# Optimization experiments

Measured on AMD Instinct MI355X. Metric: run time of the kernel, lower is better.

Reference implementation:

```python
import jax, jax.numpy as jnp
import numpy as np

B, S, D, H = 4, 2048, 1024, 16
DK = D // H
NEG = -1.0e9

def setup_inputs() -> dict:
    key = jax.random.key(0)
    ks = jax.random.split(key, 9)
    scale = 1.0 / np.sqrt(D)
    x = jax.random.normal(ks[0], (B, S, D), dtype=jnp.float32)
    # causal mask: positions with mask==0 are filled with -1e9
    mask = jnp.tril(jnp.ones((S, S), dtype=jnp.int32))[None, None]  # [1,1,S,S]
    Wq = jax.random.normal(ks[1], (D, D), dtype=jnp.float32) * scale
    bq = jax.random.normal(ks[2], (D,), dtype=jnp.float32) * 0.01
    Wk = jax.random.normal(ks[3], (D, D), dtype=jnp.float32) * scale
    bk = jax.random.normal(ks[4], (D,), dtype=jnp.float32) * 0.01
    Wv = jax.random.normal(ks[5], (D, D), dtype=jnp.float32) * scale
    bv = jax.random.normal(ks[6], (D,), dtype=jnp.float32) * 0.01
    Wo = jax.random.normal(ks[7], (D, D), dtype=jnp.float32) * scale
    bo = jax.random.normal(ks[8], (D,), dtype=jnp.float32) * 0.01
    return {"x": x, "mask": mask, "Wq": Wq, "bq": bq, "Wk": Wk, "bk": bk,
            "Wv": Wv, "bv": bv, "Wo": Wo, "bo": bo}

def reference(x, mask, Wq, bq, Wk, bk, Wv, bv, Wo, bo):
    Bb, Ss, Dd = x.shape
    q = (x @ Wq.T + bq).reshape(Bb, Ss, H, DK).transpose(0, 2, 1, 3)  # [B,H,S,DK]
    k = (x @ Wk.T + bk).reshape(Bb, Ss, H, DK).transpose(0, 2, 1, 3)
    v = (x @ Wv.T + bv).reshape(Bb, Ss, H, DK).transpose(0, 2, 1, 3)
    scaled = jnp.einsum('bhqd,bhkd->bhqk', q, k) / jnp.sqrt(jnp.float32(DK))
    scaled = jnp.where(mask == 0, jnp.float32(NEG), scaled)
    attn = jax.nn.softmax(scaled, axis=-1)  # dropout prob = 0 -> identity
    vals = jnp.einsum('bhqk,bhkd->bhqd', attn, v)  # [B,H,S,DK]
    vals = vals.transpose(0, 2, 1, 3).reshape(Bb, Ss, H * DK)
    out = vals @ Wo.T + bo
    return out
```

## Files before the change

kernel.cpp:

```cpp
#include <hip/hip_runtime.h>
#include <hip/hip_bf16.h>
#include <cstdint>

#define B_ 4
#define S_ 2048
#define D_ 1024
#define H_ 16
#define DK_ 64

typedef _Float16 h8 __attribute__((ext_vector_type(8)));
typedef _Float16 h4 __attribute__((ext_vector_type(4)));
typedef float f32x4 __attribute__((ext_vector_type(4)));
typedef float f32x16 __attribute__((ext_vector_type(16)));
typedef unsigned int u32x4 __attribute__((ext_vector_type(4)));

__device__ __forceinline__ void gload16(const void* src, void* lds) {
  __builtin_amdgcn_global_load_lds((const __attribute__((address_space(1))) void*)src,
                                   (__attribute__((address_space(3))) void*)lds, 16, 0, 0);
}

__global__ __launch_bounds__(256) void conv_all(
    const float* __restrict__ x,
    const float* __restrict__ Wq, const float* __restrict__ Wk,
    const float* __restrict__ Wv, const float* __restrict__ Wo,
    const float* __restrict__ bq, const float* __restrict__ bk,
    const float* __restrict__ bv,
    _Float16* __restrict__ xb, _Float16* __restrict__ wqkv,
    _Float16* __restrict__ wo, float* __restrict__ bqkv) {
  const int bid = blockIdx.x, tid = threadIdx.x;
  if (bid < 4096) {
    int base = (bid * 256 + tid) * 8;
    h8 o;
#pragma unroll
    for (int j = 0; j < 8; ++j) o[j] = (_Float16)x[base + j];
    *(h8*)(xb + base) = o;
  } else {
    int i = (bid - 4096) * 256 + tid;
    int seg = i >> 17, r = i & 131071;
    const float* src = seg == 0 ? Wq : seg == 1 ? Wk : seg == 2 ? Wv : Wo;
    int base = r * 8;
    h8 o;
#pragma unroll
    for (int j = 0; j < 8; ++j) o[j] = (_Float16)src[base + j];
    if (seg < 3)
      *(h8*)(wqkv + (size_t)seg * 1048576 + base) = o;
    else
      *(h8*)(wo + base) = o;
    if (i < 768) {
      int bsel = i >> 8, k = (i & 255) * 4;
      const float* bs = bsel == 0 ? bq : bsel == 1 ? bk : bv;
      float4 v = *(const float4*)(bs + k);
      *(float4*)(bqkv + bsel * 1024 + k) = v;
    }
  }
}

template <int MODE>
__global__ __launch_bounds__(256) void gemm_nt(const _Float16* __restrict__ A,
                                               const _Float16* __restrict__ Bw,
                                               const float* __restrict__ bias,
                                               void* __restrict__ Cout,
                                               _Float16* __restrict__ Vt) {
  constexpr int K = D_;
  __shared__ unsigned short lds[2 * 128 * 64];
  char* ldsA = (char*)lds;
  char* ldsB = (char*)(lds + 128 * 64);

  const int tid = threadIdx.x;
  const int w = tid >> 6, lane = tid & 63, g = lane >> 4, c = lane & 15;
  const int wr = w >> 1, wc = w & 1;
  const int bn = blockIdx.x;
  const int bm = blockIdx.y;

  f32x4 acc[4][4] = {};

  const int srow = tid >> 3;
  const int scolsw = ((tid & 7) * 16) ^ ((srow & 7) << 4);
  const char* Ab = (const char*)(A + (size_t)bm * 128 * K);
  const char* Bb = (const char*)(Bw + (size_t)bn * 128 * K);
  const char* Asrc[4];
  const char* Bsrc[4];
#pragma unroll
  for (int j = 0; j < 4; ++j) {
    int row = j * 32 + srow;
    Asrc[j] = Ab + (size_t)row * (K * 2) + scolsw;
    Bsrc[j] = Bb + (size_t)row * (K * 2) + scolsw;
  }
  char* dstA = ldsA + w * 1024;
  char* dstB = ldsB + w * 1024;

  for (int k0 = 0; k0 < K; k0 += 64) {
    __syncthreads();
#pragma unroll
    for (int j = 0; j < 4; ++j) {
      gload16(Asrc[j] + k0 * 2, dstA + j * 4096);
      gload16(Bsrc[j] + k0 * 2, dstB + j * 4096);
    }
    __syncthreads();
#pragma unroll
    for (int kk = 0; kk < 2; ++kk) {
      h8 a[4], b[4];
#pragma unroll
      for (int mi = 0; mi < 4; ++mi) {
        int row = wr * 64 + mi * 16 + c;
        int off = row * 128 + kk * 64 + g * 16;
        a[mi] = *(const h8*)(ldsA + (off ^ ((row & 7) << 4)));
      }
#pragma unroll
      for (int ni = 0; ni < 4; ++ni) {
        int row = wc * 64 + ni * 16 + c;
        int off = row * 128 + kk * 64 + g * 16;
        b[ni] = *(const h8*)(ldsB + (off ^ ((row & 7) << 4)));
      }
      __builtin_amdgcn_s_setprio(1);
#pragma unroll
      for (int mi = 0; mi < 4; ++mi)
#pragma unroll
        for (int ni = 0; ni < 4; ++ni)
          acc[mi][ni] = __builtin_amdgcn_mfma_f32_16x16x32_f16(a[mi], b[ni], acc[mi][ni], 0, 0, 0);
      __builtin_amdgcn_s_setprio(0);
    }
  }

  if (MODE == 0 && bn >= 16) {
#pragma unroll
    for (int mi = 0; mi < 4; ++mi)
#pragma unroll
      for (int ni = 0; ni < 4; ++ni) {
        int m0 = bm * 128 + wr * 64 + mi * 16 + g * 4;
        int n = bn * 128 + wc * 64 + ni * 16 + c;
        float bb = bias[n];
        h4 v4;
#pragma unroll
        for (int r = 0; r < 4; ++r) v4[r] = (_Float16)(acc[mi][ni][r] + bb);
        int bI = m0 >> 11, sI = m0 & 2047;
        int dk = n & 63, hh = (n >> 6) & 15;
        *(h4*)(Vt + (((size_t)(bI * 16 + hh) * 64 + dk) * 2048 + sI)) = v4;
      }
  } else {
#pragma unroll
    for (int mi = 0; mi < 4; ++mi)
#pragma unroll
      for (int ni = 0; ni < 4; ++ni)
#pragma unroll
        for (int r = 0; r < 4; ++r) {
          int m = bm * 128 + wr * 64 + mi * 16 + g * 4 + r;
          int n = bn * 128 + wc * 64 + ni * 16 + c;
          float v = acc[mi][ni][r] + bias[n];
          if (MODE == 0) {
            int which = n >> 10, nn = n & 1023;
            int bI = m >> 11, sI = m & 2047, hI = nn >> 6, dkI = nn & 63;
            ((_Float16*)Cout)[(size_t)which * 8388608 +
                              (((size_t)bI * H_ + hI) * S_ + sI) * DK_ + dkI] = (_Float16)v;
          } else {
            ((float*)Cout)[(size_t)m * D_ + n] = v;
          }
        }
  }
}

__global__ __launch_bounds__(128) void attn_fwd(const _Float16* __restrict__ Q,
                                                const _Float16* __restrict__ K,
                                                const _Float16* __restrict__ Vt,
                                                _Float16* __restrict__ vals) {
  __shared__ char lds[2 * 16384];

  const int tid = threadIdx.x;
  const int w = tid >> 6;
  const int lane = tid & 63;
  const int l31 = lane & 31, hi = lane >> 5;
  const int bid = blockIdx.x;
  const int pi = bid >> 6;
  const int bh = bid & 63;
  const int bI = bh >> 4, hI = bh & 15;

  const char* Qb = (const char*)(Q + (size_t)bh * S_ * DK_);
  const char* Kb = (const char*)(K + (size_t)bh * S_ * DK_);
  const char* Vtb = (const char*)(Vt + (size_t)bh * DK_ * S_);

  const int srow = tid >> 3;
  const int scol = (tid & 7) * 16;
  int offK[4], offV[4];
#pragma unroll
  for (int j = 0; j < 4; ++j) {
    int row = j * 16 + srow;
    int colsw = scol ^ ((row & 7) << 4);
    offK[j] = row * 128 + colsw;
    offV[j] = row * 4096 + colsw;
  }

  int rdo[4];
#pragma unroll
  for (int ks = 0; ks < 4; ++ks)
    rdo[ks] = l31 * 128 + ((ks * 32 + hi * 16) ^ ((l31 & 7) << 4));

  const _Float16 qsc = (_Float16)(0.125f * 1.44269504f);

  for (int phase = 0; phase < 2; ++phase) {
    const int p64 = (phase == 0) ? pi : 31 - pi;
    const int qs32 = p64 * 2 + w;
    const int nt = p64 + 1;

    h8 qf[4];
#pragma unroll
    for (int ks = 0; ks < 4; ++ks) {
      h8 v = *(const h8*)(Qb + (size_t)(qs32 * 32 + l31) * 128 + ks * 32 + hi * 16);
#pragma unroll
      for (int j = 0; j < 8; ++j) v[j] *= qsc;
      qf[ks] = v;
    }

    f32x16 o[2] = {};
    float m_ = -1e30f, l_ = 0.f;

#pragma unroll
    for (int j = 0; j < 4; ++j) {
      gload16(Kb + offK[j], lds + j * 2048 + w * 1024);
      gload16(Vtb + offV[j], lds + 8192 + j * 2048 + w * 1024);
    }
    __syncthreads();

    for (int t = 0; t < nt; ++t) {
      const int cur = t & 1;
      const char* ldsb = lds + cur * 16384;
      if (t + 1 < nt) {
        const size_t kvo = (size_t)(t + 1) * 64;
        char* nb = lds + (cur ^ 1) * 16384;
#pragma unroll
        for (int j = 0; j < 4; ++j) {
          gload16(Kb + kvo * 128 + offK[j], nb + j * 2048 + w * 1024);
          gload16(Vtb + kvo * 2 + offV[j], nb + 8192 + j * 2048 + w * 1024);
        }
      }

      const bool diag = (t == nt - 1);
      const bool skip1 = diag && (w == 0);

      f32x16 s0 = {}, s1 = {};
#pragma unroll
      for (int ks = 0; ks < 4; ++ks) {
        h8 k0 = *(const h8*)(ldsb + rdo[ks]);
        h8 k1 = *(const h8*)(ldsb + 4096 + rdo[ks]);
        __builtin_amdgcn_s_setprio(1);
        s0 = __builtin_amdgcn_mfma_f32_32x32x16_f16(k0, qf[ks], s0, 0, 0, 0);
        if (!skip1) s1 = __builtin_amdgcn_mfma_f32_32x32x16_f16(k1, qf[ks], s1, 0, 0, 0);
        __builtin_amdgcn_s_setprio(0);
      }

      if (diag) {
        if (w == 0) {
#pragma unroll
          for (int r = 0; r < 16; ++r) {
            int rowidx = (r & 3) + 8 * (r >> 2) + 4 * hi;
            if (rowidx > l31) s0[r] = -1e30f;
          }
        } else {
#pragma unroll
          for (int r = 0; r < 16; ++r) {
            int rowidx = (r & 3) + 8 * (r >> 2) + 4 * hi;
            if (rowidx > l31) s1[r] = -1e30f;
          }
        }
      }

      float t8[8];
#pragma unroll
      for (int j = 0; j < 8; ++j) t8[j] = fmaxf(s0[2 * j], s0[2 * j + 1]);
      if (!skip1)
#pragma unroll
        for (int j = 0; j < 8; ++j) t8[j] = fmaxf(t8[j], fmaxf(s1[2 * j], s1[2 * j + 1]));
      float t4a = fmaxf(t8[0], t8[1]), t4b = fmaxf(t8[2], t8[3]);
      float t4c = fmaxf(t8[4], t8[5]), t4d = fmaxf(t8[6], t8[7]);
      float pmax = fmaxf(fmaxf(t4a, t4b), fmaxf(t4c, t4d));

      if (!__all(pmax <= m_ + 8.f)) {
        float rm = fmaxf(pmax, __shfl_xor(pmax, 32));
        float mn = fmaxf(m_, rm);
        float al = __builtin_amdgcn_exp2f(m_ - mn);
        m_ = mn;
        l_ *= al;
#pragma unroll
        for (int r = 0; r < 16; ++r) {
          float av = __shfl(al, (r & 3) + 8 * (r >> 2) + 4 * hi);
          o[0][r] *= av;
          o[1][r] *= av;
        }
      }

      unsigned int u0[8], u1[8];
      float rsa = 0.f, rsb = 0.f;
#pragma unroll
      for (int j = 0; j < 8; ++j) {
        float e0 = __builtin_amdgcn_exp2f(s0[2 * j] - m_);
        float e1 = __builtin_amdgcn_exp2f(s0[2 * j + 1] - m_);
        rsa += e0 + e1;
        u0[j] = __builtin_bit_cast(unsigned int, __builtin_amdgcn_cvt_pkrtz(e0, e1));
      }
      if (!skip1) {
#pragma unroll
        for (int j = 0; j < 8; ++j) {
          float e0 = __builtin_amdgcn_exp2f(s1[2 * j] - m_);
          float e1 = __builtin_amdgcn_exp2f(s1[2 * j + 1] - m_);
          rsb += e0 + e1;
          u1[j] = __builtin_bit_cast(unsigned int, __builtin_amdgcn_cvt_pkrtz(e0, e1));
        }
      }
      l_ += rsa + rsb;

      h8 pa0[2], pa1[2];
#pragma unroll
      for (int b = 0; b < 2; ++b) {
        unsigned int ua = u0[4 * b], ub = u0[4 * b + 1];
        unsigned int uc = u0[4 * b + 2], ud = u0[4 * b + 3];
        unsigned int va = hi ? ua : uc, vb = hi ? ub : ud;
        unsigned int xa = __shfl_xor(va, 32), xb = __shfl_xor(vb, 32);
        u32x4 q = {hi ? xa : ua, hi ? xb : ub, hi ? uc : xa, hi ? ud : xb};
        pa0[b] = __builtin_bit_cast(h8, q);
      }
      if (!skip1) {
#pragma unroll
        for (int b = 0; b < 2; ++b) {
          unsigned int ua = u1[4 * b], ub = u1[4 * b + 1];
          unsigned int uc = u1[4 * b + 2], ud = u1[4 * b + 3];
          unsigned int va = hi ? ua : uc, vb = hi ? ub : ud;
          unsigned int xa = __shfl_xor(va, 32), xb = __shfl_xor(vb, 32);
          u32x4 q = {hi ? xa : ua, hi ? xb : ub, hi ? uc : xa, hi ? ud : xb};
          pa1[b] = __builtin_bit_cast(h8, q);
        }
      }

#pragma unroll
      for (int x = 0; x < 2; ++x) {
#pragma unroll
        for (int kvs = 0; kvs < 4; ++kvs) {
          int ni = kvs >> 1, b = kvs & 1;
          if (skip1 && ni == 1) continue;
          h8 vf = *(const h8*)(ldsb + 8192 + x * 4096 + rdo[kvs]);
          h8 pa = ni ? pa1[b] : pa0[b];
          __builtin_amdgcn_s_setprio(1);
          o[x] = __builtin_amdgcn_mfma_f32_32x32x16_f16(pa, vf, o[x], 0, 0, 0);
          __builtin_amdgcn_s_setprio(0);
        }
      }

      __syncthreads();
    }

    float lt = l_ + __shfl_xor(l_, 32);
    float linv = 1.0f / lt;
#pragma unroll
    for (int r = 0; r < 16; ++r) {
      int qidx = (r & 3) + 8 * (r >> 2) + 4 * hi;
      float inv = __shfl(linv, qidx);
      int qrow = qs32 * 32 + qidx;
      size_t rowoff = ((size_t)bI * S_ + qrow) * D_ + hI * 64 + l31;
      vals[rowoff] = (_Float16)(o[0][r] * inv);
      vals[rowoff + 32] = (_Float16)(o[1][r] * inv);
    }
  }
}

extern "C" void kernel_launch(void* const* d_in, const int* in_sizes, int n_in,
                              void* d_out, int out_size, void* d_ws, size_t ws_size,
                              hipStream_t stream) {
  const float* x  = (const float*)d_in[0];
  const float* Wq = (const float*)d_in[2];
  const float* bq = (const float*)d_in[3];
  const float* Wk = (const float*)d_in[4];
  const float* bk = (const float*)d_in[5];
  const float* Wv = (const float*)d_in[6];
  const float* bv = (const float*)d_in[7];
  const float* Wo = (const float*)d_in[8];
  const float* bo = (const float*)d_in[9];
  float* out = (float*)d_out;

  char* ws = (char*)d_ws;
  size_t off = 0;
  auto alloc = [&](size_t bytes) {
    char* p = ws + off;
    off += (bytes + 255) & ~(size_t)255;
    return p;
  };
  _Float16* xb   = (_Float16*)alloc((size_t)B_ * S_ * D_ * 2);
  _Float16* wqkv = (_Float16*)alloc((size_t)3 * D_ * D_ * 2);
  _Float16* wob  = (_Float16*)alloc((size_t)D_ * D_ * 2);
  float*    bqkv = (float*)alloc((size_t)3 * D_ * 4);
  _Float16* qkvw = (_Float16*)alloc((size_t)2 * B_ * H_ * S_ * DK_ * 2);
  _Float16* Vtw  = (_Float16*)alloc((size_t)B_ * H_ * S_ * DK_ * 2);
  _Float16* valw = (_Float16*)alloc((size_t)B_ * S_ * D_ * 2);

  conv_all<<<6144, 256, 0, stream>>>(x, Wq, Wk, Wv, Wo, bq, bk, bv, xb, wqkv, wob, bqkv);

  gemm_nt<0><<<dim3(24, 64), 256, 0, stream>>>(xb, wqkv, bqkv, qkvw, Vtw);

  attn_fwd<<<1024, 128, 0, stream>>>(qkvw, qkvw + (size_t)8388608, Vtw, valw);

  gemm_nt<1><<<dim3(8, 64), 256, 0, stream>>>(valw, wob, bo, out, nullptr);
}
```

Baseline: 209.0 us.

## Widen attention blocks to 8 waves sharing each staged K/V tile

The attention kernel now launches 256 blocks of 512 threads, each covering 256 query rows (8 waves of 32 rows), instead of 1024 blocks of 128 threads. Each K/V tile staged in LDS is reused by 8 waves instead of 2, which cuts global/L2 traffic per query and the number of staging loads per thread. Waves whose query range lies entirely before the current KV tile skip the compute but still join every barrier. This adds idle waves inside a block on the causal tail and leaves fewer blocks for the 256 CUs, which risks load imbalance.

Result: faster. 176.9 us (-15.4%).

```diff
diff --git a/kernel.cpp b/kernel.cpp
--- a/kernel.cpp
+++ b/kernel.cpp
@@ -159,7 +159,7 @@
   }
 }
 
-__global__ __launch_bounds__(128) void attn_fwd(const _Float16* __restrict__ Q,
+__global__ __launch_bounds__(512) void attn_fwd(const _Float16* __restrict__ Q,
                                                 const _Float16* __restrict__ K,
                                                 const _Float16* __restrict__ Vt,
                                                 _Float16* __restrict__ vals) {
@@ -179,32 +179,31 @@
   const char* Vtb = (const char*)(Vt + (size_t)bh * DK_ * S_);
 
   const int srow = tid >> 3;
-  const int scol = (tid & 7) * 16;
-  int offK[4], offV[4];
-#pragma unroll
-  for (int j = 0; j < 4; ++j) {
-    int row = j * 16 + srow;
-    int colsw = scol ^ ((row & 7) << 4);
-    offK[j] = row * 128 + colsw;
-    offV[j] = row * 4096 + colsw;
-  }
+  const int colsw = ((tid & 7) * 16) ^ ((srow & 7) << 4);
+  const int offK = srow * 128 + colsw;
+  const int offV = srow * 4096 + colsw;
 
   int rdo[4];
 #pragma unroll
   for (int ks = 0; ks < 4; ++ks)
     rdo[ks] = l31 * 128 + ((ks * 32 + hi * 16) ^ ((l31 & 7) << 4));
 
+  auto stage = [&](char* buf, int kv0) {
+    gload16(Kb + (size_t)kv0 * 128 + offK, buf + w * 1024);
+    gload16(Vtb + (size_t)kv0 * 2 + offV, buf + 8192 + w * 1024);
+  };
+
   const _Float16 qsc = (_Float16)(0.125f * 1.44269504f);
 
   for (int phase = 0; phase < 2; ++phase) {
-    const int p64 = (phase == 0) ? pi : 31 - pi;
-    const int qs32 = p64 * 2 + w;
-    const int nt = p64 + 1;
+    const int sup = (phase == 0) ? pi : 7 - pi;
+    const int qw = sup * 8 + w;
+    const int nt = 4 * sup + 4;
 
     h8 qf[4];
 #pragma unroll
     for (int ks = 0; ks < 4; ++ks) {
-      h8 v = *(const h8*)(Qb + (size_t)(qs32 * 32 + l31) * 128 + ks * 32 + hi * 16);
+      h8 v = *(const h8*)(Qb + (size_t)(qw * 32 + l31) * 128 + ks * 32 + hi * 16);
 #pragma unroll
       for (int j = 0; j < 8; ++j) v[j] *= qsc;
       qf[ks] = v;
@@ -213,133 +212,125 @@
     f32x16 o[2] = {};
     float m_ = -1e30f, l_ = 0.f;
 
-#pragma unroll
-    for (int j = 0; j < 4; ++j) {
-      gload16(Kb + offK[j], lds + j * 2048 + w * 1024);
-      gload16(Vtb + offV[j], lds + 8192 + j * 2048 + w * 1024);
-    }
+    stage(lds, 0);
     __syncthreads();
 
     for (int t = 0; t < nt; ++t) {
       const int cur = t & 1;
       const char* ldsb = lds + cur * 16384;
-      if (t + 1 < nt) {
-        const size_t kvo = (size_t)(t + 1) * 64;
-        char* nb = lds + (cur ^ 1) * 16384;
-#pragma unroll
-        for (int j = 0; j < 4; ++j) {
-          gload16(Kb + kvo * 128 + offK[j], nb + j * 2048 + w * 1024);
-          gload16(Vtb + kvo * 2 + offV[j], nb + 8192 + j * 2048 + w * 1024);
-        }
-      }
-
-      const bool diag = (t == nt - 1);
-      const bool skip1 = diag && (w == 0);
-
-      f32x16 s0 = {}, s1 = {};
-#pragma unroll
-      for (int ks = 0; ks < 4; ++ks) {
-        h8 k0 = *(const h8*)(ldsb + rdo[ks]);
-        h8 k1 = *(const h8*)(ldsb + 4096 + rdo[ks]);
-        __builtin_amdgcn_s_setprio(1);
-        s0 = __builtin_amdgcn_mfma_f32_32x32x16_f16(k0, qf[ks], s0, 0, 0, 0);
-        if (!skip1) s1 = __builtin_amdgcn_mfma_f32_32x32x16_f16(k1, qf[ks], s1, 0, 0, 0);
-        __builtin_amdgcn_s_setprio(0);
-      }
-
-      if (diag) {
-        if (w == 0) {
+      if (t + 1 < nt) stage(lds + (cur ^ 1) * 16384, (t + 1) * 64);
+
+      const int rel = qw - 2 * t;
+      if (rel >= 0) {
+        const bool have1 = (rel >= 1);
+
+        f32x16 s0 = {}, s1 = {};
+#pragma unroll
+        for (int ks = 0; ks < 4; ++ks) {
+          h8 k0 = *(const h8*)(ldsb + rdo[ks]);
+          __builtin_amdgcn_s_setprio(1);
+          s0 = __builtin_amdgcn_mfma_f32_32x32x16_f16(k0, qf[ks], s0, 0, 0, 0);
+          __builtin_amdgcn_s_setprio(0);
+          if (have1) {
+            h8 k1 = *(const h8*)(ldsb + 4096 + rdo[ks]);
+            __builtin_amdgcn_s_setprio(1);
+            s1 = __builtin_amdgcn_mfma_f32_32x32x16_f16(k1, qf[ks], s1, 0, 0, 0);
+            __builtin_amdgcn_s_setprio(0);
+          }
+        }
+
+        if (rel == 0) {
 #pragma unroll
           for (int r = 0; r < 16; ++r) {
             int rowidx = (r & 3) + 8 * (r >> 2) + 4 * hi;
             if (rowidx > l31) s0[r] = -1e30f;
           }
-        } else {
+        } else if (rel == 1) {
 #pragma unroll
           for (int r = 0; r < 16; ++r) {
             int rowidx = (r & 3) + 8 * (r >> 2) + 4 * hi;
             if (rowidx > l31) s1[r] = -1e30f;
           }
         }
-      }
-
-      float t8[8];
-#pragma unroll
-      for (int j = 0; j < 8; ++j) t8[j] = fmaxf(s0[2 * j], s0[2 * j + 1]);
-      if (!skip1)
-#pragma unroll
-        for (int j = 0; j < 8; ++j) t8[j] = fmaxf(t8[j], fmaxf(s1[2 * j], s1[2 * j + 1]));
-      float t4a = fmaxf(t8[0], t8[1]), t4b = fmaxf(t8[2], t8[3]);
-      float t4c = fmaxf(t8[4], t8[5]), t4d = fmaxf(t8[6], t8[7]);
-      float pmax = fmaxf(fmaxf(t4a, t4b), fmaxf(t4c, t4d));
-
-      if (!__all(pmax <= m_ + 8.f)) {
-        float rm = fmaxf(pmax, __shfl_xor(pmax, 32));
-        float mn = fmaxf(m_, rm);
-        float al = __builtin_amdgcn_exp2f(m_ - mn);
-        m_ = mn;
-        l_ *= al;
-#pragma unroll
-        for (int r = 0; r < 16; ++r) {
-          float av = __shfl(al, (r & 3) + 8 * (r >> 2) + 4 * hi);
-          o[0][r] *= av;
-          o[1][r] *= av;
-        }
-      }
-
-      unsigned int u0[8], u1[8];
-      float rsa = 0.f, rsb = 0.f;
-#pragma unroll
-      for (int j = 0; j < 8; ++j) {
-        float e0 = __builtin_amdgcn_exp2f(s0[2 * j] - m_);
-        float e1 = __builtin_amdgcn_exp2f(s0[2 * j + 1] - m_);
-        rsa += e0 + e1;
-        u0[j] = __builtin_bit_cast(unsigned int, __builtin_amdgcn_cvt_pkrtz(e0, e1));
-      }
-      if (!skip1) {
+
+        float t8[8];
+#pragma unroll
+        for (int j = 0; j < 8; ++j) t8[j] = fmaxf(s0[2 * j], s0[2 * j + 1]);
+        if (have1)
+#pragma unroll
+          for (int j = 0; j < 8; ++j) t8[j] = fmaxf(t8[j], fmaxf(s1[2 * j], s1[2 * j + 1]));
+        float t4a = fmaxf(t8[0], t8[1]), t4b = fmaxf(t8[2], t8[3]);
+        float t4c = fmaxf(t8[4], t8[5]), t4d = fmaxf(t8[6], t8[7]);
+        float pmax = fmaxf(fmaxf(t4a, t4b), fmaxf(t4c, t4d));
+
+        if (!__all(pmax <= m_ + 8.f)) {
+          float rm = fmaxf(pmax, __shfl_xor(pmax, 32));
+          float mn = fmaxf(m_, rm);
+          float al = __builtin_amdgcn_exp2f(m_ - mn);
+          m_ = mn;
+          l_ *= al;
+#pragma unroll
+          for (int r = 0; r < 16; ++r) {
+            float av = __shfl(al, (r & 3) + 8 * (r >> 2) + 4 * hi);
+            o[0][r] *= av;
+            o[1][r] *= av;
+          }
+        }
+
+        unsigned int u0[8], u1[8];
+        float rsa = 0.f, rsb = 0.f;
 #pragma unroll
         for (int j = 0; j < 8; ++j) {
-          float e0 = __builtin_amdgcn_exp2f(s1[2 * j] - m_);
-          float e1 = __builtin_amdgcn_exp2f(s1[2 * j + 1] - m_);
-          rsb += e0 + e1;
-          u1[j] = __builtin_bit_cast(unsigned int, __builtin_amdgcn_cvt_pkrtz(e0, e1));
-        }
-      }
-      l_ += rsa + rsb;
-
-      h8 pa0[2], pa1[2];
-#pragma unroll
-      for (int b = 0; b < 2; ++b) {
-        unsigned int ua = u0[4 * b], ub = u0[4 * b + 1];
-        unsigned int uc = u0[4 * b + 2], ud = u0[4 * b + 3];
-        unsigned int va = hi ? ua : uc, vb = hi ? ub : ud;
-        unsigned int xa = __shfl_xor(va, 32), xb = __shfl_xor(vb, 32);
-        u32x4 q = {hi ? xa : ua, hi ? xb : ub, hi ? uc : xa, hi ? ud : xb};
-        pa0[b] = __builtin_bit_cast(h8, q);
-      }
-      if (!skip1) {
+          float e0 = __builtin_amdgcn_exp2f(s0[2 * j] - m_);
+          float e1 = __builtin_amdgcn_exp2f(s0[2 * j + 1] - m_);
+          rsa += e0 + e1;
+          u0[j] = __builtin_bit_cast(unsigned int, __builtin_amdgcn_cvt_pkrtz(e0, e1));
+        }
+        if (have1) {
+#pragma unroll
+          for (int j = 0; j < 8; ++j) {
+            float e0 = __builtin_amdgcn_exp2f(s1[2 * j] - m_);
+            float e1 = __builtin_amdgcn_exp2f(s1[2 * j + 1] - m_);
+            rsb += e0 + e1;
+            u1[j] = __builtin_bit_cast(unsigned int, __builtin_amdgcn_cvt_pkrtz(e0, e1));
+          }
+        }
+        l_ += rsa + rsb;
+
+        h8 pa0[2], pa1[2];
 #pragma unroll
         for (int b = 0; b < 2; ++b) {
-          unsigned int ua = u1[4 * b], ub = u1[4 * b + 1];
-          unsigned int uc = u1[4 * b + 2], ud = u1[4 * b + 3];
+          unsigned int ua = u0[4 * b], ub = u0[4 * b + 1];
+          unsigned int uc = u0[4 * b + 2], ud = u0[4 * b + 3];
           unsigned int va = hi ? ua : uc, vb = hi ? ub : ud;
           unsigned int xa = __shfl_xor(va, 32), xb = __shfl_xor(vb, 32);
           u32x4 q = {hi ? xa : ua, hi ? xb : ub, hi ? uc : xa, hi ? ud : xb};
-          pa1[b] = __builtin_bit_cast(h8, q);
-        }
-      }
-
-#pragma unroll
-      for (int x = 0; x < 2; ++x) {
-#pragma unroll
-        for (int kvs = 0; kvs < 4; ++kvs) {
-          int ni = kvs >> 1, b = kvs & 1;
-          if (skip1 && ni == 1) continue;
-          h8 vf = *(const h8*)(ldsb + 8192 + x * 4096 + rdo[kvs]);
-          h8 pa = ni ? pa1[b] : pa0[b];
-          __builtin_amdgcn_s_setprio(1);
-          o[x] = __builtin_amdgcn_mfma_f32_32x32x16_f16(pa, vf, o[x], 0, 0, 0);
-          __builtin_amdgcn_s_setprio(0);
+          pa0[b] = __builtin_bit_cast(h8, q);
+        }
+        if (have1) {
+#pragma unroll
+          for (int b = 0; b < 2; ++b) {
+            unsigned int ua = u1[4 * b], ub = u1[4 * b + 1];
+            unsigned int uc = u1[4 * b + 2], ud = u1[4 * b + 3];
+            unsigned int va = hi ? ua : uc, vb = hi ? ub : ud;
+            unsigned int xa = __shfl_xor(va, 32), xb = __shfl_xor(vb, 32);
+            u32x4 q = {hi ? xa : ua, hi ? xb : ub, hi ? uc : xa, hi ? ud : xb};
+            pa1[b] = __builtin_bit_cast(h8, q);
+          }
+        }
+
+#pragma unroll
+        for (int x = 0; x < 2; ++x) {
+#pragma unroll
+          for (int kvs = 0; kvs < 4; ++kvs) {
+            int ni = kvs >> 1, b = kvs & 1;
+            if (!have1 && ni == 1) continue;
+            h8 vf = *(const h8*)(ldsb + 8192 + x * 4096 + rdo[kvs]);
+            h8 pa = ni ? pa1[b] : pa0[b];
+            __builtin_amdgcn_s_setprio(1);
+            o[x] = __builtin_amdgcn_mfma_f32_32x32x16_f16(pa, vf, o[x], 0, 0, 0);
+            __builtin_amdgcn_s_setprio(0);
+          }
         }
       }
 
@@ -352,7 +343,7 @@
     for (int r = 0; r < 16; ++r) {
       int qidx = (r & 3) + 8 * (r >> 2) + 4 * hi;
       float inv = __shfl(linv, qidx);
-      int qrow = qs32 * 32 + qidx;
+      int qrow = qw * 32 + qidx;
       size_t rowoff = ((size_t)bI * S_ + qrow) * D_ + hI * 64 + l31;
       vals[rowoff] = (_Float16)(o[0][r] * inv);
       vals[rowoff + 32] = (_Float16)(o[1][r] * inv);
@@ -393,7 +384,7 @@
 
   gemm_nt<0><<<dim3(24, 64), 256, 0, stream>>>(xb, wqkv, bqkv, qkvw, Vtw);
 
-  attn_fwd<<<1024, 128, 0, stream>>>(qkvw, qkvw + (size_t)8388608, Vtw, valw);
+  attn_fwd<<<256, 512, 0, stream>>>(qkvw, qkvw + (size_t)8388608, Vtw, valw);
 
   gemm_nt<1><<<dim3(8, 64), 256, 0, stream>>>(valw, wob, bo, out, nullptr);
 }
```
